# Kernel tuning notes

Hardware: AMD Instinct MI355X
Metric: run time of the kernel (lower is better)

Reference implementation:

```python
import jax, jax.numpy as jnp
import numpy as np

B, S, DIM, H = 2, 2048, 1024, 16
HD = DIM // H  # head dim = 64


def setup_inputs() -> dict:
    key = jax.random.key(0)
    ks = jax.random.split(key, 10)
    scale = 1.0 / np.sqrt(DIM)
    x = jax.random.normal(ks[0], (B, S, DIM), dtype=jnp.float32)
    # per-head projection weights stacked over heads: [H, DIM, HD]
    Wq = jax.random.normal(ks[1], (H, DIM, HD), dtype=jnp.float32) * scale
    bq = jax.random.normal(ks[2], (H, HD), dtype=jnp.float32) * 0.01
    Wk = jax.random.normal(ks[3], (H, DIM, HD), dtype=jnp.float32) * scale
    bk = jax.random.normal(ks[4], (H, HD), dtype=jnp.float32) * 0.01
    Wv = jax.random.normal(ks[5], (H, DIM, HD), dtype=jnp.float32) * scale
    bv = jax.random.normal(ks[6], (H, HD), dtype=jnp.float32) * 0.01
    # output linear: [DIM, DIM]
    Wo = jax.random.normal(ks[7], (DIM, DIM), dtype=jnp.float32) * scale
    bo = jax.random.normal(ks[8], (DIM,), dtype=jnp.float32) * 0.01
    return {"x": x, "Wq": Wq, "bq": bq, "Wk": Wk, "bk": bk,
            "Wv": Wv, "bv": bv, "Wo": Wo, "bo": bo}


def reference(x, Wq, bq, Wk, bk, Wv, bv, Wo, bo):
    # per-head projections: [B, H, S, HD]
    q = jnp.einsum('bsd,hde->bhse', x, Wq) + bq[None, :, None, :]
    k = jnp.einsum('bsd,hde->bhse', x, Wk) + bk[None, :, None, :]
    v = jnp.einsum('bsd,hde->bhse', x, Wv) + bv[None, :, None, :]
    # causal attention scores: [B, H, S, S], scaled by sqrt(head_dim)
    scores = jnp.einsum('bhse,bhte->bhst', q, k) / jnp.sqrt(jnp.float32(HD))
    causal = jnp.tril(jnp.ones((S, S), dtype=bool))
    scores = jnp.where(causal[None, None], scores, -jnp.inf)
    attn = jax.nn.softmax(scores, axis=-1)
    out = jnp.einsum('bhst,bhte->bhse', attn, v)  # [B, H, S, HD]
    # concat heads in order -> [B, S, DIM]
    out = out.transpose(0, 2, 1, 3).reshape(B, S, DIM)
    return out @ Wo + bo
```

## Files before the change

### kernel.cpp

```cpp
#include <hip/hip_runtime.h>

typedef _Float16 half8 __attribute__((ext_vector_type(8)));
typedef _Float16 half4 __attribute__((ext_vector_type(4)));
typedef float f32x4 __attribute__((ext_vector_type(4)));

#define MFMA32(a, b, c) __builtin_amdgcn_mfma_f32_16x16x32_f16((a), (b), (c), 0, 0, 0)
#define MFMA16(a, b, c) __builtin_amdgcn_mfma_f32_16x16x16f16((a), (b), (c), 0, 0, 0)

static constexpr int Bc = 2, Sc = 2048, DIMc = 1024, Hc = 16, HDc = 64;
static constexpr int Mc = Bc * Sc;
static constexpr int NQKV = 3 * DIMc;

__device__ __forceinline__ void gl_lds16(const _Float16* g, _Float16* l) {
  __builtin_amdgcn_global_load_lds(
      (const __attribute__((address_space(1))) void*)g,
      (__attribute__((address_space(3))) void*)l, 16, 0, 0);
}


__global__ __launch_bounds__(256) void k_prep_all(
    const float* __restrict__ x, const float* __restrict__ Wq,
    const float* __restrict__ Wk, const float* __restrict__ Wv,
    const float* __restrict__ Wo, _Float16* __restrict__ xh,
    _Float16* __restrict__ WallT, _Float16* __restrict__ WoT) {
  __shared__ float Ls[64 * 65];
  const int bx = blockIdx.x, tid = threadIdx.x;
  if (bx < 2048) {
    const int i = bx * 256 + tid;
    const float4* xf = (const float4*)x;
    float4 a = xf[i * 2], b = xf[i * 2 + 1];
    half8 hv;
    hv[0] = (_Float16)a.x; hv[1] = (_Float16)a.y;
    hv[2] = (_Float16)a.z; hv[3] = (_Float16)a.w;
    hv[4] = (_Float16)b.x; hv[5] = (_Float16)b.y;
    hv[6] = (_Float16)b.z; hv[7] = (_Float16)b.w;
    *(half8*)&xh[(size_t)i * 8] = hv;
    return;
  }
  int b2 = bx - 2048;
  if (b2 < 768) {
    const int dt = b2 & 15, ph = b2 >> 4;
    const int p = ph >> 4, h = ph & 15;
    const float* W = (p == 0) ? Wq : (p == 1) ? Wk : Wv;
    for (int c = tid; c < 4096; c += 256) {
      int dr = c >> 6, e = c & 63;
      Ls[e * 65 + dr] = W[h * 65536 + (dt * 64 + dr) * 64 + e];
    }
    __syncthreads();
    for (int c = tid; c < 4096; c += 256) {
      int e = c >> 6, dr = c & 63;
      WallT[(size_t)(p * 1024 + h * 64 + e) * 1024 + dt * 64 + dr] = (_Float16)Ls[e * 65 + dr];
    }
  } else {
    int b3 = b2 - 768;
    const int dt = b3 & 15, nt = b3 >> 4;
    for (int c = tid; c < 4096; c += 256) {
      int dr = c >> 6, nl = c & 63;
      Ls[nl * 65 + dr] = Wo[(dt * 64 + dr) * 1024 + nt * 64 + nl];
    }
    __syncthreads();
    for (int c = tid; c < 4096; c += 256) {
      int nl = c >> 6, dr = c & 63;
      WoT[(size_t)(nt * 64 + nl) * 1024 + dt * 64 + dr] = (_Float16)Ls[nl * 65 + dr];
    }
  }
}


#define STAGE_WP(buf, kk0)                                                     \
  {                                                                            \
    const int r_ = lane >> 2;                                                  \
    const int c_ = ((lane & 3) ^ ((r_ >> 1) & 3)) * 8;                         \
    for (int it = 0; it < 4; ++it)                                             \
      gl_lds16(&Arow[(size_t)(it * 16 + r_) * DIMc + (kk0) + c_],              \
               &SH[wave][buf][0][it * 512]);                                   \
    for (int it = 0; it < 4; ++it)                                             \
      gl_lds16(&Brow[(size_t)(it * 16 + r_) * DIMc + (kk0) + c_],              \
               &SH[wave][buf][1][it * 512]);                                   \
  }

#define COMPUTE_WP(buf)                                                        \
  {                                                                            \
    half8 af[4], bf[4];                                                        \
    for (int i = 0; i < 4; i++)                                                \
      af[i] = *(const half8*)&SH[wave][buf][0][(i * 16 + mr) * 32 + sl];       \
    for (int i = 0; i < 4; i++)                                                \
      bf[i] = *(const half8*)&SH[wave][buf][1][(i * 16 + mr) * 32 + sl];       \
    for (int i = 0; i < 4; i++)                                                \
      for (int j = 0; j < 4; j++) acc[i][j] = MFMA32(af[i], bf[j], acc[i][j]); \
  }

#define GEMM_CORE()                                                            \
  __shared__ _Float16 SH[4][2][2][64 * 32];        \
  const int tid = threadIdx.x;                                                 \
  const int lane = tid & 63, wave = tid >> 6;                                  \
  const int quad = lane >> 4, mr = lane & 15;                                  \
  const int sl = (quad ^ ((mr >> 1) & 3)) * 8;                                 \
  const int wm = wave >> 1, wn = wave & 1;                                     \
  const _Float16* Arow = A + (size_t)(m0 + wm * 64) * DIMc;                    \
  const _Float16* Brow = Bt + (size_t)(n0 + wn * 64) * DIMc;                   \
  f32x4 acc[4][4];                                                             \
  for (int i = 0; i < 4; i++)                                                  \
    for (int j = 0; j < 4; j++) acc[i][j] = f32x4{0.f, 0.f, 0.f, 0.f};         \
  STAGE_WP(0, 0)                                                               \
  for (int k0 = 0; k0 < DIMc; k0 += 64) {                                      \
    STAGE_WP(1, k0 + 32)                                                       \
    asm volatile("s_waitcnt vmcnt(8)" ::: "memory");                           \
    __builtin_amdgcn_sched_barrier(0);                                         \
    COMPUTE_WP(0)                                                              \
    __builtin_amdgcn_sched_barrier(0);                                         \
    if (k0 + 64 < DIMc) {                                                      \
      STAGE_WP(0, k0 + 64)                                                     \
      asm volatile("s_waitcnt vmcnt(8)" ::: "memory");                         \
    } else {                                                                   \
      asm volatile("s_waitcnt vmcnt(0)" ::: "memory");                         \
    }                                                                          \
    __builtin_amdgcn_sched_barrier(0);                                         \
    COMPUTE_WP(1)                                                              \
    __builtin_amdgcn_sched_barrier(0);                                         \
  }

__global__ __launch_bounds__(256, 2) void k_gemm_qkv(
    const _Float16* __restrict__ xh, const _Float16* __restrict__ WallT,
    const float* __restrict__ bq, const float* __restrict__ bk,
    const float* __restrict__ bv, _Float16* __restrict__ qh,
    _Float16* __restrict__ kh, _Float16* __restrict__ vT) {
  const int id = blockIdx.x;
  const bool qkrole = id < 512;
  const _Float16* A;
  const _Float16* Bt;
  int m0, n0;
  if (qkrole) {
    A = xh; Bt = WallT;
    n0 = (id & 15) * 128; m0 = (id >> 4) * 128;
  } else {
    int j = id - 512;
    A = WallT + (size_t)2048 * DIMc; Bt = xh;
    n0 = (j & 31) * 128; m0 = (j >> 5) * 128;
  }
  GEMM_CORE()
  if (qkrole) {
    for (int i = 0; i < 4; i++) {
      for (int j = 0; j < 4; j++) {
        int col = n0 + wn * 64 + j * 16 + mr;
        int p = col >> 10, rem = col & 1023;
        const float* bias = p ? bk : bq;
        _Float16* dst = p ? kh : qh;
        float bb = bias[rem];
        int h = rem >> 6, e = rem & 63;
        for (int r = 0; r < 4; r++) {
          int row = m0 + wm * 64 + i * 16 + quad * 4 + r;
          int b = row >> 11, s = row & 2047;
          dst[(((size_t)(b * Hc + h)) * Sc + s) * HDc + e] = (_Float16)(acc[i][j][r] + bb);
        }
      }
    }
  } else {
    for (int i = 0; i < 4; i++) {
      int rowb = m0 + wm * 64 + i * 16 + quad * 4;
      for (int j = 0; j < 4; j++) {
        int col = n0 + wn * 64 + j * 16 + mr;
        int b = col >> 11, s = col & 2047;
        for (int r = 0; r < 4; r++) {
          int row = rowb + r;
          vT[(size_t)(b * 1024 + row) * Sc + s] = (_Float16)(acc[i][j][r] + bv[row]);
        }
      }
    }
  }
}

__global__ __launch_bounds__(256, 2) void k_gemm_out(
    const _Float16* __restrict__ A, const _Float16* __restrict__ Bt,
    const float* __restrict__ bo, float* __restrict__ out) {
  const int m0 = blockIdx.y * 128, n0 = blockIdx.x * 128;
  GEMM_CORE()
  for (int i = 0; i < 4; i++) {
    for (int j = 0; j < 4; j++) {
      int col = n0 + wn * 64 + j * 16 + mr;
      float bb = bo[col];
      for (int r = 0; r < 4; r++) {
        int row = m0 + wm * 64 + i * 16 + quad * 4 + r;
        out[(size_t)row * DIMc + col] = acc[i][j][r] + bb;
      }
    }
  }
}


__global__ __launch_bounds__(256, 2) void k_attn(
    const _Float16* __restrict__ qg, const _Float16* __restrict__ kg,
    const _Float16* __restrict__ vTg, _Float16* __restrict__ att) {
  const int bid = blockIdx.x;
  const int qt = 31 - (bid >> 5);
  const int bh = bid & 31;
  const int b = bh >> 4, h = bh & 15;
  const int tid = threadIdx.x, w = tid >> 6, lane = tid & 63;
  const int quad = lane >> 4, mr = lane & 15, m7 = mr & 7, m3 = mr & 3;
  const size_t base = (size_t)bh * (Sc * HDc);
  const _Float16* Kg = kg + base;
  const _Float16* Vg = vTg + ((size_t)b * 1024 + h * 64) * Sc;

  __shared__ _Float16 KV[4][2][2][2048];
  __shared__ float Lsh[4][64];

  const int q0 = qt * 64;
  const int ntt = 2 * qt + 2;
  const int myn = (w < ntt) ? ((ntt - 1 - w) >> 2) + 1 : 0;

  const _Float16 qsc = (_Float16)(0.125f * 1.44269504f);
  half8 aq[4][2];
  for (int qf = 0; qf < 4; ++qf)
    for (int c = 0; c < 2; ++c) {
      half8 v = *(const half8*)&qg[base + (size_t)(q0 + qf * 16 + mr) * 64 + c * 32 + quad * 8];
      for (int j = 0; j < 8; ++j) v[j] = v[j] * qsc;
      aq[qf][c] = v;
    }

  f32x4 o[4][4];
  f32x4 ol[4];
  for (int nf = 0; nf < 4; ++nf)
    for (int qf = 0; qf < 4; ++qf) o[nf][qf] = f32x4{0.f, 0.f, 0.f, 0.f};
  for (int qf = 0; qf < 4; ++qf) ol[qf] = f32x4{0.f, 0.f, 0.f, 0.f};
  const half4 ones = {(_Float16)1.f, (_Float16)1.f, (_Float16)1.f, (_Float16)1.f};

#define STAGE32(dst, tt)                                                       \
  {                                                                            \
    const _Float16* ks = Kg + (size_t)(tt) * 2048;                             \
    const _Float16* vs = Vg + (tt) * 32;                                       \
    for (int it = 0; it < 4; ++it) {                                           \
      int idx = it * 64 + lane;                                                \
      int row = idx >> 3, scb = (idx & 7) ^ (row & 7);                         \
      gl_lds16(ks + (size_t)row * 64 + scb * 8, (dst) + it * 512);             \
    }                                                                          \
    for (int it = 0; it < 4; ++it) {                                           \
      int idx = it * 64 + lane;                                                \
      int row = idx >> 2, scb = (idx & 3) ^ (row & 3);                         \
      gl_lds16(vs + (size_t)row * Sc + scb * 8, (dst) + 2048 + it * 512);      \
    }                                                                          \
  }

  if (myn > 0) STAGE32(&KV[w][0][0][0], w)
  asm volatile("s_waitcnt vmcnt(0)" ::: "memory");

  for (int i = 0; i < myn; ++i) {
    const int t = w + 4 * i;
    const _Float16* Kc = &KV[w][i & 1][0][0];
    const _Float16* Vc = &KV[w][i & 1][1][0];
    if (i + 1 < myn) STAGE32(&KV[w][(i + 1) & 1][0][0], t + 4)

    __builtin_amdgcn_s_setprio(1);
    const int dg = (t - 2 * qt) * 32;
    half4 pf[4][2];
    for (int kf = 0; kf < 2; ++kf) {
      const int r0 = (kf * 16 + mr) * 64;
      half8 k0 = *(const half8*)&Kc[r0 + ((quad ^ m7) * 8)];
      half8 k1 = *(const half8*)&Kc[r0 + (((quad ^ 4) ^ m7) * 8)];
      for (int qf = 0; qf < 4; ++qf) {
        f32x4 z = {0.f, 0.f, 0.f, 0.f};
        z = MFMA32(k0, aq[qf][0], z);
        z = MFMA32(k1, aq[qf][1], z);
        half4 pp;
        const int kvr = dg + kf * 16 + quad * 4;
        for (int r = 0; r < 4; ++r) {
          float p = __builtin_amdgcn_exp2f(z[r]);
          if (kvr + r > qf * 16 + mr) p = 0.f;
          pp[r] = (_Float16)p;
        }
        pf[qf][kf] = pp;
      }
    }

    for (int nf = 0; nf < 4; ++nf) {
      const int rb = (nf * 16 + mr) * 32;
      for (int kc = 0; kc < 2; ++kc) {
        int ch = kc * 2 + (quad >> 1);
        half4 vv = *(const half4*)&Vc[rb + ((ch ^ m3) * 8) + (quad & 1) * 4];
        for (int qf = 0; qf < 4; ++qf)
          o[nf][qf] = MFMA16(vv, pf[qf][kc], o[nf][qf]);
      }
    }
    for (int kc = 0; kc < 2; ++kc)
      for (int qf = 0; qf < 4; ++qf) ol[qf] = MFMA16(ones, pf[qf][kc], ol[qf]);
    __builtin_amdgcn_s_setprio(0);

    asm volatile("s_waitcnt vmcnt(0)" ::: "memory");
  }

  float* Osh = (float*)&KV[0][0][0][0];
  for (int nf = 0; nf < 4; ++nf)
    for (int qf = 0; qf < 4; ++qf)
      for (int r = 0; r < 4; ++r)
        Osh[w * 4096 + (nf * 16 + quad * 4 + r) * 64 + qf * 16 + mr] = o[nf][qf][r];
  if (quad == 0)
    for (int qf = 0; qf < 4; ++qf) Lsh[w][qf * 16 + mr] = ol[qf][0];
  __syncthreads();

  const int q = tid & 63, e0 = (tid >> 6) * 16;
  const float linv = 1.0f / (Lsh[0][q] + Lsh[1][q] + Lsh[2][q] + Lsh[3][q]);
  half8 o0, o1;
  for (int e = 0; e < 8; ++e) {
    float s = Osh[(e0 + e) * 64 + q] + Osh[4096 + (e0 + e) * 64 + q] +
              Osh[8192 + (e0 + e) * 64 + q] + Osh[12288 + (e0 + e) * 64 + q];
    o0[e] = (_Float16)(s * linv);
  }
  for (int e = 8; e < 16; ++e) {
    float s = Osh[(e0 + e) * 64 + q] + Osh[4096 + (e0 + e) * 64 + q] +
              Osh[8192 + (e0 + e) * 64 + q] + Osh[12288 + (e0 + e) * 64 + q];
    o1[e - 8] = (_Float16)(s * linv);
  }
  const size_t orow = ((size_t)(b * Sc + q0 + q)) * DIMc + h * 64 + e0;
  *(half8*)&att[orow] = o0;
  *(half8*)&att[orow + 8] = o1;
#undef STAGE32
}


extern "C" void kernel_launch(void* const* d_in, const int* in_sizes, int n_in,
                              void* d_out, int out_size, void* d_ws, size_t ws_size,
                              hipStream_t stream) {
  const float* x  = (const float*)d_in[0];
  const float* Wq = (const float*)d_in[1];
  const float* bq = (const float*)d_in[2];
  const float* Wk = (const float*)d_in[3];
  const float* bk = (const float*)d_in[4];
  const float* Wv = (const float*)d_in[5];
  const float* bv = (const float*)d_in[6];
  const float* Wo = (const float*)d_in[7];
  const float* bo = (const float*)d_in[8];
  float* out = (float*)d_out;

  _Float16* p = (_Float16*)d_ws;
  _Float16* xh    = p; p += (size_t)Mc * DIMc;
  _Float16* WallT = p; p += (size_t)NQKV * DIMc;
  _Float16* WoT   = p; p += (size_t)DIMc * DIMc;
  _Float16* qh    = p; p += (size_t)Bc * Hc * Sc * HDc;
  _Float16* kh    = p; p += (size_t)Bc * Hc * Sc * HDc;
  _Float16* vT    = p; p += (size_t)Bc * Hc * Sc * HDc;
  _Float16* atth  = p;

  k_prep_all<<<2048 + 768 + 256, 256, 0, stream>>>(x, Wq, Wk, Wv, Wo, xh, WallT, WoT);
  k_gemm_qkv<<<768, 256, 0, stream>>>(xh, WallT, bq, bk, bv, qh, kh, vT);
  k_attn<<<1024, 256, 0, stream>>>(qh, kh, vT, atth);
  k_gemm_out<<<dim3(DIMc / 128, Mc / 128), 256, 0, stream>>>(atth, WoT, bo, out);
}
```

Measured before the change: 187.9 us.

## Use cooperative block-shared LDS tiles for QKV GEMM instead of per-wave staging

The QKV projection GEMM now stages shared 128x32 A and B tiles into LDS cooperatively across all four waves, with double buffering and block barriers. Before, each wave loaded its own 64-row slices privately. Each block now fetches each tile once from global memory, roughly halving global/L2 traffic, and the smaller LDS footprint lets launch bounds rise to 3 blocks per CU. The cost is two workgroup barriers per 32-wide k step and a shorter k-step per barrier, which may expose latency. The output GEMM keeps the per-wave path.

Result: faster. 181.3 us (median of 2 runs) (-3.5%).

```diff
diff --git a/kernel.cpp b/kernel.cpp
--- a/kernel.cpp
+++ b/kernel.cpp
@@ -67,6 +67,55 @@
 }
 
 
+#define STAGE_AB(buf, kk0)                                                     \
+    for (int it = 0; it < 2; ++it) {                                           \
+      int idx = it * 256 + tid;                                                \
+      int row = idx >> 2, scb = (idx & 3) ^ ((row >> 1) & 3);                  \
+      gl_lds16(&A[(size_t)(m0 + row) * DIMc + (kk0) + scb * 8],                \
+               &As[buf][(it * 256 + wave * 64) * 8]);                          \
+    }                                                                          \
+    for (int it = 0; it < 2; ++it) {                                           \
+      int idx = it * 256 + tid;                                                \
+      int row = idx >> 2, scb = (idx & 3) ^ ((row >> 1) & 3);                  \
+      gl_lds16(&Bt[(size_t)(n0 + row) * DIMc + (kk0) + scb * 8],               \
+               &Bs[buf][(it * 256 + wave * 64) * 8]);                          \
+    }
+
+#define GEMM_CORE_COOP()                                                       \
+  __shared__ _Float16 As[2][128 * 32];                                         \
+  __shared__ _Float16 Bs[2][128 * 32];                                         \
+  const int tid = threadIdx.x;                                                 \
+  const int lane = tid & 63, wave = tid >> 6;                                  \
+  const int quad = lane >> 4, mr = lane & 15;                                  \
+  const int sl = quad ^ ((mr >> 1) & 3);                                       \
+  const int wm = wave >> 1, wn = wave & 1;                                     \
+  f32x4 acc[4][4];                                                             \
+  for (int i = 0; i < 4; i++)                                                  \
+    for (int j = 0; j < 4; j++) acc[i][j] = f32x4{0.f, 0.f, 0.f, 0.f};         \
+  STAGE_AB(0, 0)                                                               \
+  for (int k0 = 0; k0 < DIMc; k0 += 32) {                                      \
+    const int cur = (k0 >> 5) & 1;                                             \
+    if (k0 + 32 < DIMc) {                                                      \
+      STAGE_AB(cur ^ 1, k0 + 32)                                               \
+      asm volatile("s_waitcnt vmcnt(4)" ::: "memory");                         \
+    } else {                                                                   \
+      asm volatile("s_waitcnt vmcnt(0)" ::: "memory");                         \
+    }                                                                          \
+    __builtin_amdgcn_s_barrier();                                              \
+    __builtin_amdgcn_sched_barrier(0);                                         \
+    half8 af[4], bf[4];                                                        \
+    for (int i = 0; i < 4; i++)                                                \
+      af[i] = *(const half8*)&As[cur][(wm * 64 + i * 16 + mr) * 32 + sl * 8];  \
+    for (int i = 0; i < 4; i++)                                                \
+      bf[i] = *(const half8*)&Bs[cur][(wn * 64 + i * 16 + mr) * 32 + sl * 8];  \
+    for (int i = 0; i < 4; i++)                                                \
+      for (int j = 0; j < 4; j++) acc[i][j] = MFMA32(af[i], bf[j], acc[i][j]); \
+    asm volatile("s_waitcnt lgkmcnt(0)" ::: "memory");                         \
+    __builtin_amdgcn_s_barrier();                                              \
+    __builtin_amdgcn_sched_barrier(0);                                         \
+  }
+
+
 #define STAGE_WP(buf, kk0)                                                     \
   {                                                                            \
     const int r_ = lane >> 2;                                                  \
@@ -90,7 +139,7 @@
       for (int j = 0; j < 4; j++) acc[i][j] = MFMA32(af[i], bf[j], acc[i][j]); \
   }
 
-#define GEMM_CORE()                                                            \
+#define GEMM_CORE_WP()                                                         \
   __shared__ _Float16 SH[4][2][2][64 * 32];        \
   const int tid = threadIdx.x;                                                 \
   const int lane = tid & 63, wave = tid >> 6;                                  \
@@ -120,7 +169,7 @@
     __builtin_amdgcn_sched_barrier(0);                                         \
   }
 
-__global__ __launch_bounds__(256, 2) void k_gemm_qkv(
+__global__ __launch_bounds__(256, 3) void k_gemm_qkv(
     const _Float16* __restrict__ xh, const _Float16* __restrict__ WallT,
     const float* __restrict__ bq, const float* __restrict__ bk,
     const float* __restrict__ bv, _Float16* __restrict__ qh,
@@ -138,7 +187,7 @@
     A = WallT + (size_t)2048 * DIMc; Bt = xh;
     n0 = (j & 31) * 128; m0 = (j >> 5) * 128;
   }
-  GEMM_CORE()
+  GEMM_CORE_COOP()
   if (qkrole) {
     for (int i = 0; i < 4; i++) {
       for (int j = 0; j < 4; j++) {
@@ -174,7 +223,7 @@
     const _Float16* __restrict__ A, const _Float16* __restrict__ Bt,
     const float* __restrict__ bo, float* __restrict__ out) {
   const int m0 = blockIdx.y * 128, n0 = blockIdx.x * 128;
-  GEMM_CORE()
+  GEMM_CORE_WP()
   for (int i = 0; i < 4; i++) {
     for (int j = 0; j < 4; j++) {
       int col = n0 + wn * 64 + j * 16 + mr;
```
